# Kernel tuning notes

Hardware: AMD Instinct MI355X
Metric: run time of the kernel (lower is better)

Reference implementation:

```python
import jax, jax.numpy as jnp
import numpy as np

# Mamba2 hyperparams (from config['block'][0])
D_MODEL = 512
D_STATE = 64
D_CONV = 4
EXPAND = 2
HEADDIM = 64
D_INNER = EXPAND * D_MODEL          # 1024
NHEADS = D_INNER // HEADDIM         # 16
CONV_DIM = D_INNER + 2 * D_STATE    # 1152 (x, B, C share the depthwise conv)
D_IN_PROJ = 2 * D_INNER + 2 * D_STATE + NHEADS  # z | xBC | dt
EPS = 1e-5
BATCH, SEQLEN = 2, 4096


def setup_inputs() -> dict:
    key = jax.random.key(0)
    ks = jax.random.split(key, 10)
    x = jax.random.normal(ks[0], (BATCH, SEQLEN, D_MODEL), dtype=jnp.float32)
    W_in = jax.random.normal(ks[1], (D_MODEL, D_IN_PROJ), dtype=jnp.float32) * 0.02
    conv_w = jax.random.normal(ks[2], (CONV_DIM, 1, D_CONV), dtype=jnp.float32) * 0.2
    conv_b = jax.random.normal(ks[3], (CONV_DIM,), dtype=jnp.float32) * 0.02
    dt_bias = jax.random.uniform(ks[4], (NHEADS,), minval=-4.0, maxval=-1.0, dtype=jnp.float32)
    A_log = jnp.log(jax.random.uniform(ks[5], (NHEADS,), minval=1.0, maxval=16.0, dtype=jnp.float32))
    D = jax.random.normal(ks[6], (NHEADS,), dtype=jnp.float32) * 0.5 + 1.0
    norm_weight = jnp.ones((D_INNER,), dtype=jnp.float32)
    W_out = jax.random.normal(ks[7], (D_INNER, D_MODEL), dtype=jnp.float32) * 0.02
    return {"x": x, "W_in": W_in, "conv_w": conv_w, "conv_b": conv_b,
            "dt_bias": dt_bias, "A_log": A_log, "D": D,
            "norm_weight": norm_weight, "W_out": W_out}


def _mamba2_forward(x, W_in, conv_w, conv_b, dt_bias, A_log, D, norm_weight, W_out):
    b, l, _ = x.shape
    zxbcdt = x @ W_in                                      # (b, l, D_IN_PROJ)
    z = zxbcdt[..., :D_INNER]                              # gate branch
    xBC = zxbcdt[..., D_INNER:D_INNER + CONV_DIM]
    dt = zxbcdt[..., D_INNER + CONV_DIM:]                  # (b, l, h)

    # depthwise causal conv1d over sequence, then SiLU
    xBC_ncw = jnp.transpose(xBC, (0, 2, 1))                # (b, c, l)
    xBC_ncw = jax.lax.conv_general_dilated(
        xBC_ncw, conv_w, window_strides=(1,), padding=[(D_CONV - 1, 0)],
        dimension_numbers=("NCW", "OIW", "NCW"), feature_group_count=CONV_DIM)
    xBC_ncw = xBC_ncw + conv_b[None, :, None]
    xBC = jax.nn.silu(jnp.transpose(xBC_ncw, (0, 2, 1)))   # (b, l, c)

    x_ssm = xBC[..., :D_INNER].reshape(b, l, NHEADS, HEADDIM)  # (b,l,h,p)
    B = xBC[..., D_INNER:D_INNER + D_STATE]                    # (b,l,n)
    C = xBC[..., D_INNER + D_STATE:]                           # (b,l,n)

    dt = jax.nn.softplus(dt + dt_bias)                     # (b,l,h)
    A = -jnp.exp(A_log)                                    # (h,)
    dA = jnp.exp(dt * A)                                   # (b,l,h) discrete decay

    # selective scan: state s has shape (b, h, p, n)
    def step(s, inp):
        dA_t, dt_t, x_t, B_t, C_t = inp                    # (b,h),(b,h),(b,h,p),(b,n),(b,n)
        dBx = (dt_t[..., None] * x_t)[..., None] * B_t[:, None, None, :]
        s = s * dA_t[..., None, None] + dBx
        y_t = jnp.einsum("bhpn,bn->bhp", s, C_t)
        return s, y_t

    s0 = jnp.zeros((b, NHEADS, HEADDIM, D_STATE), dtype=x.dtype)
    xs = (jnp.moveaxis(dA, 1, 0), jnp.moveaxis(dt, 1, 0),
          jnp.moveaxis(x_ssm, 1, 0), jnp.moveaxis(B, 1, 0), jnp.moveaxis(C, 1, 0))
    _, ys = jax.lax.scan(step, s0, xs)                     # ys: (l,b,h,p)
    y = jnp.moveaxis(ys, 0, 1)                             # (b,l,h,p)

    y = y + D[None, None, :, None] * x_ssm                 # skip term
    y = y.reshape(b, l, D_INNER)

    # gated RMSNorm (norm after gating, mamba2 default)
    y = y * jax.nn.silu(z)
    var = jnp.mean(jnp.square(y), axis=-1, keepdims=True)
    y = y * jax.lax.rsqrt(var + EPS) * norm_weight

    return y @ W_out                                       # (b, l, d_model)


def reference(x, W_in, conv_w, conv_b, dt_bias, A_log, D, norm_weight, W_out):
    return _mamba2_forward(x, W_in, conv_w, conv_b, dt_bias, A_log, D, norm_weight, W_out)
```

## Files before the change

### kernel.cpp

```cpp
#include <hip/hip_runtime.h>
#include <hip/hip_bf16.h>

#define BATCH   2
#define SEQ     4096
#define DMODEL  512
#define DINNER  1024
#define DSTATE  64
#define NHEADS  16
#define HEADDIM 64
#define CONVDIM 1152
#define NPROJ   2192
#define NPROJ_PAD 2304
#define MROWS   (BATCH*SEQ)
#define QCH     64
#define NCHUNK  (SEQ/QCH)

typedef short bf16x8 __attribute__((ext_vector_type(8)));
typedef float f32x4  __attribute__((ext_vector_type(4)));
using bf16 = __hip_bfloat16;
typedef unsigned short ushort_t;
typedef unsigned int   uint_t;

__device__ __forceinline__ float sigmoidf_(float x) { return 1.f / (1.f + __expf(-x)); }
__device__ __forceinline__ float bf2f(ushort_t u) { return __uint_as_float((uint_t)u << 16); }
__device__ __forceinline__ ushort_t f2bfu(float f) {
    bf16 h = __float2bfloat16(f);
    return *(ushort_t*)&h;
}
__device__ __forceinline__ void bf8_to_f(const ushort_t* __restrict__ p, float* __restrict__ f) {
    uint4 u = *(const uint4*)p;
    f[0] = __uint_as_float((u.x & 0xFFFFu) << 16);
    f[1] = __uint_as_float(u.x & 0xFFFF0000u);
    f[2] = __uint_as_float((u.y & 0xFFFFu) << 16);
    f[3] = __uint_as_float(u.y & 0xFFFF0000u);
    f[4] = __uint_as_float((u.z & 0xFFFFu) << 16);
    f[5] = __uint_as_float(u.z & 0xFFFF0000u);
    f[6] = __uint_as_float((u.w & 0xFFFFu) << 16);
    f[7] = __uint_as_float(u.w & 0xFFFF0000u);
}
__device__ __forceinline__ uint4 f8_to_bf(const float* __restrict__ f) {
    union { ushort_t s[8]; uint4 u; } r;
#pragma unroll
    for (int i = 0; i < 8; i++) r.s[i] = f2bfu(f[i]);
    return r.u;
}

__device__ __forceinline__ void gload_lds16(const ushort_t* g, ushort_t* l)
{
    __builtin_amdgcn_global_load_lds(
        (const __attribute__((address_space(1))) void*)g,
        (__attribute__((address_space(3)))       void*)l,
        16, 0, 0);
}

__global__ __launch_bounds__(256, 4)
void prep_k(const float* __restrict__ x, ushort_t* __restrict__ xb,
            const float* __restrict__ W_in, ushort_t* __restrict__ WinT,
            const float* __restrict__ W_out, ushort_t* __restrict__ WoutT,
            const float* __restrict__ nw)
{
    __shared__ __align__(16) ushort_t tile[32][33];
    const int bid = blockIdx.x, tid = threadIdx.x;
    if (bid < 2048) {
        int i = bid * 256 + tid;
        float f[8];
        *(float4*)(f + 0) = ((const float4*)x)[i * 2 + 0];
        *(float4*)(f + 4) = ((const float4*)x)[i * 2 + 1];
        ((uint4*)xb)[i] = f8_to_bf(f);
        return;
    }
    const int tx = tid & 31, ty = tid >> 5;
    const float* in; ushort_t* out; int R, C, Cpad; const float* sv;
    int bx, by;
    if (bid < 3200) {
        int b2 = bid - 2048;
        bx = b2 % (NPROJ_PAD / 32); by = b2 / (NPROJ_PAD / 32);
        in = W_in; out = WinT; R = DMODEL; C = NPROJ; Cpad = NPROJ_PAD; sv = nullptr;
    } else {
        int b3 = bid - 3200;
        bx = b3 % (DMODEL / 32); by = b3 / (DMODEL / 32);
        in = W_out; out = WoutT; R = DINNER; C = DMODEL; Cpad = DMODEL; sv = nw;
    }
    int c0 = bx * 32, r0 = by * 32;
#pragma unroll
    for (int i = 0; i < 32; i += 8) {
        int r = r0 + ty + i, c = c0 + tx;
        float v = (r < R && c < C) ? in[(size_t)r * C + c] : 0.f;
        if (sv && r < R) v *= sv[r];
        tile[ty + i][tx] = f2bfu(v);
    }
    __syncthreads();
#pragma unroll
    for (int i = 0; i < 32; i += 8) {
        int orow = c0 + ty + i, ocol = r0 + tx;
        if (orow < Cpad && ocol < R) out[(size_t)orow * R + ocol] = tile[tx][ty + i];
    }
}

__global__ __launch_bounds__(256, 4)
void conv_k(const ushort_t* __restrict__ xpbc, const ushort_t* __restrict__ xpre,
            const float* __restrict__ cw, const float* __restrict__ cb,
            ushort_t* __restrict__ bcc, ushort_t* __restrict__ xs)
{
    const int bid = blockIdx.x, tid = threadIdx.x;
    if (bid < 512) {
        int idx = bid * 256 + tid;
        int row = idx >> 4, c8 = (idx & 15) * 8;
        int l = row & (SEQ - 1);
        float acc[8];
#pragma unroll
        for (int i = 0; i < 8; i++) acc[i] = cb[1024 + c8 + i];
#pragma unroll
        for (int j = 0; j < 4; j++) {
            int ll = l - 3 + j;
            if (ll >= 0) {
                float v[8];
                bf8_to_f(xpbc + (size_t)(row - 3 + j) * 128 + c8, v);
#pragma unroll
                for (int i = 0; i < 8; i++) acc[i] += cw[(1024 + c8 + i) * 4 + j] * v[i];
            }
        }
#pragma unroll
        for (int i = 0; i < 8; i++) { float v = acc[i]; acc[i] = v * sigmoidf_(v); }
        *(uint4*)(bcc + (size_t)row * 128 + c8) = f8_to_bf(acc);
        return;
    }
    const int b2 = bid - 512;
    const int gx = b2 & 127, b = b2 >> 7;
    const int c8 = (tid & 127) * 8;
    const int rh = tid >> 7;
    const int l0 = gx * 32 + rh * 16;
    float w[4][8], cbv[8];
#pragma unroll
    for (int i = 0; i < 8; i++) {
        cbv[i] = cb[c8 + i];
        float4 wv = *(const float4*)(cw + (size_t)(c8 + i) * 4);
        w[0][i] = wv.x; w[1][i] = wv.y; w[2][i] = wv.z; w[3][i] = wv.w;
    }
    float win[3][8];
#pragma unroll
    for (int j = 0; j < 3; j++) {
        int ll = l0 - 3 + j;
        if (ll >= 0) bf8_to_f(xpre + ((size_t)b * SEQ + ll) * 1024 + c8, win[j]);
        else {
#pragma unroll
            for (int i = 0; i < 8; i++) win[j][i] = 0.f;
        }
    }
#pragma unroll 4
    for (int r = 0; r < 16; r++) {
        int l = l0 + r;
        float cur[8], o[8];
        bf8_to_f(xpre + ((size_t)b * SEQ + l) * 1024 + c8, cur);
#pragma unroll
        for (int i = 0; i < 8; i++) {
            float a = cbv[i] + w[0][i] * win[0][i] + w[1][i] * win[1][i]
                             + w[2][i] * win[2][i] + w[3][i] * cur[i];
            o[i] = a * sigmoidf_(a);
        }
        *(uint4*)(xs + ((size_t)b * SEQ + l) * 1024 + c8) = f8_to_bf(o);
#pragma unroll
        for (int i = 0; i < 8; i++) { win[0][i] = win[1][i]; win[1][i] = win[2][i]; win[2][i] = cur[i]; }
    }
}

template<int MODE>
__global__ __launch_bounds__(256, MODE == 1 ? 4 : 3)
void gemm_k(const ushort_t* __restrict__ A, const ushort_t* __restrict__ Bt,
            ushort_t* __restrict__ zbuf, ushort_t* __restrict__ xpx,
            ushort_t* __restrict__ xpbc, float* __restrict__ dtv,
            float* __restrict__ dalog, const float* __restrict__ dt_b,
            const float* __restrict__ A_log, float* __restrict__ outf,
            int M, int N, int K)
{
    constexpr int TN = (MODE == 1) ? 64 : 128;
    constexpr int NJ = TN / 32;
    constexpr int SC = 132;
    constexpr int SMEM_ELTS = (MODE == 1) ? (128 * 64 + TN * 64) : (128 * SC);
    __shared__ __align__(16) ushort_t smem[SMEM_ELTS];
    ushort_t* As = smem;
    ushort_t* Bs = smem + 128 * 64;
    ushort_t* Cs = smem;

    const int tid  = threadIdx.x;
    const int wave = tid >> 6, lane = tid & 63;
    const int quad = lane >> 4, l16 = lane & 15;
    const int wm = (wave >> 1) * 64, wn = (wave & 1) * (TN / 2);

    const int GX = gridDim.x;
    int lin = blockIdx.y * GX + blockIdx.x;
    const int cpx = (GX * gridDim.y) >> 3;
    lin = (lin & 7) * cpx + (lin >> 3);
    const int m0 = (lin / GX) * 128, n0 = (lin % GX) * TN;

    const int srow = lane >> 3;
    const int scol = (lane & 7) * 8;
    const ushort_t* ag = A  + (size_t)(m0 + wave * 32       + srow) * K + scol;
    const ushort_t* bg = Bt + (size_t)(n0 + wave * (TN / 4) + srow) * K + scol;
    ushort_t* al = As + wave * 32 * 64;
    ushort_t* bl = Bs + wave * (TN / 4) * 64;

    f32x4 acc[4][NJ];
#pragma unroll
    for (int i = 0; i < 4; i++)
#pragma unroll
        for (int j = 0; j < NJ; j++) acc[i][j] = (f32x4){0.f, 0.f, 0.f, 0.f};
    float ssq4[4] = {0.f, 0.f, 0.f, 0.f};

    for (int k0 = 0; k0 < K; k0 += 64) {
        __syncthreads();
#pragma unroll
        for (int j = 0; j < 4; j++)
            gload_lds16(ag + (size_t)(j * 8) * K + k0, al + j * 8 * 64);
#pragma unroll
        for (int j = 0; j < NJ; j++)
            gload_lds16(bg + (size_t)(j * 8) * K + k0, bl + j * 8 * 64);
        __syncthreads();
#pragma unroll
        for (int kk = 0; kk < 64; kk += 32) {
            bf16x8 af[4], bfr[NJ];
#pragma unroll
            for (int i = 0; i < 4; i++)
                af[i] = *(const bf16x8*)(&As[(wm + i * 16 + l16) * 64 + kk + quad * 8]);
#pragma unroll
            for (int j = 0; j < NJ; j++)
                bfr[j] = *(const bf16x8*)(&Bs[(wn + j * 16 + l16) * 64 + kk + quad * 8]);
#pragma unroll
            for (int i = 0; i < 4; i++)
#pragma unroll
                for (int j = 0; j < NJ; j++)
                    acc[i][j] = __builtin_amdgcn_mfma_f32_16x16x32_bf16(af[i], bfr[j], acc[i][j], 0, 0, 0);
            if (MODE == 1 && (wave & 1) == 0) {
#pragma unroll
                for (int i = 0; i < 4; i++)
#pragma unroll
                    for (int e = 0; e < 8; e++) {
                        float f = bf2f((ushort_t)af[i][e]);
                        ssq4[i] += f * f;
                    }
            }
        }
    }
    if (MODE == 1) {
        __syncthreads();
        float* smemf = (float*)smem;
        if ((wave & 1) == 0) {
#pragma unroll
            for (int i = 0; i < 4; i++) {
                float s = ssq4[i];
                s += __shfl_xor(s, 16, 64);
                s += __shfl_xor(s, 32, 64);
                if (quad == 0) smemf[wm + i * 16 + l16] = s;
            }
        }
        __syncthreads();
#pragma unroll
        for (int i = 0; i < 4; i++)
#pragma unroll
            for (int j = 0; j < NJ; j++) {
                int col  = n0 + wn + j * 16 + l16;
                int rowl = wm + i * 16 + quad * 4;
#pragma unroll
                for (int r = 0; r < 4; r++) {
                    float sc = rsqrtf(smemf[rowl + r] * (1.f / DINNER) + 1e-5f);
                    outf[(size_t)(m0 + rowl + r) * N + col] = acc[i][j][r] * sc;
                }
            }
    } else if (n0 == 2176) {
#pragma unroll
        for (int i = 0; i < 4; i++)
#pragma unroll
            for (int j = 0; j < NJ; j++) {
                int col = n0 + wn + j * 16 + l16;
                int rowb = m0 + wm + i * 16 + quad * 4;
                if (col < N) {
                    int hh = col - 2176;
#pragma unroll
                    for (int r = 0; r < 4; r++) {
                        float v = acc[i][j][r];
                        size_t g = (size_t)hh * MROWS + (rowb + r);
                        float raw = v + dt_b[hh];
                        float sp  = (raw > 20.f) ? raw : log1pf(__expf(raw));
                        dtv  [g] = sp;
                        dalog[g] = -__expf(A_log[hh]) * sp;
                    }
                }
            }
    } else {
        __syncthreads();
#pragma unroll
        for (int i = 0; i < 4; i++)
#pragma unroll
            for (int j = 0; j < NJ; j++)
#pragma unroll
                for (int r = 0; r < 4; r++)
                    Cs[(wm + i * 16 + quad * 4 + r) * SC + wn + j * 16 + l16] = f2bfu(acc[i][j][r]);
        __syncthreads();
        ushort_t* dst; int ld, coff;
        if (n0 < 1024)      { dst = zbuf; ld = 1024; coff = n0; }
        else if (n0 < 2048) { dst = xpx;  ld = 1024; coff = n0 - 1024; }
        else                { dst = xpbc; ld = 128;  coff = 0; }
#pragma unroll
        for (int jj = 0; jj < 8; jj++) {
            int idx = jj * 256 + tid;
            int row = idx >> 4, cq = (idx & 15) * 8;
            uint4 v = *(const uint4*)&Cs[row * SC + cq];
            *(uint4*)&dst[(size_t)(m0 + row) * ld + coff + cq] = v;
        }
    }
}

__global__ __launch_bounds__(256, 3)
void chunk_state_k(const ushort_t* __restrict__ xs, const ushort_t* __restrict__ bcc,
                   const float* __restrict__ dtv, const float* __restrict__ dalog,
                   ushort_t* __restrict__ statesT, float* __restrict__ cdecay)
{
    const int c = blockIdx.x, h = blockIdx.y, b = blockIdx.z;
    __shared__ __align__(16) ushort_t xsT[64 * 72];
    __shared__ __align__(16) ushort_t BwT[64 * 72];
    __shared__ float wc[64];
    const int tid = threadIdx.x;
    const int ts = tid >> 2, q4 = (tid & 3) * 16;
    const int l = c * QCH + ts;
    const int tswz = ts ^ ((tid & 3) << 4);
    if (tid < 64) {
        size_t gl = (size_t)h * MROWS + (size_t)b * SEQ + c * QCH + tid;
        float v = dalog[gl];
#pragma unroll
        for (int off = 1; off < 64; off <<= 1) {
            float u = __shfl_up(v, off, 64);
            if (tid >= off) v += u;
        }
        float tot = __shfl(v, 63, 64);
        wc[tid] = __expf(tot - v) * dtv[gl];
        if (tid == 63) cdecay[(c * BATCH + b) * NHEADS + h] = __expf(tot);
    }
    {
        const int ch0 = h * HEADDIM + q4;
        const ushort_t* rp = xs + ((size_t)b * SEQ + l) * 1024 + ch0;
        union { uint4 u; ushort_t s[8]; } u0, u1;
        u0.u = *(const uint4*)rp; u1.u = *(const uint4*)(rp + 8);
#pragma unroll
        for (int i = 0; i < 8; i++) {
            xsT[(q4 + i) * 72 + tswz]     = u0.s[i];
            xsT[(q4 + 8 + i) * 72 + tswz] = u1.s[i];
        }
    }
    __syncthreads();
    {
        float bv[16];
        const ushort_t* rp = bcc + ((size_t)b * SEQ + l) * 128;
        bf8_to_f(rp + q4, bv); bf8_to_f(rp + q4 + 8, bv + 8);
        const float wt = wc[ts];
#pragma unroll
        for (int i = 0; i < 16; i++) BwT[(q4 + i) * 72 + tswz] = f2bfu(bv[i] * wt);
    }
    __syncthreads();
    const int wave = tid >> 6, lane = tid & 63;
    const int quad = lane >> 4, l16 = lane & 15;
    f32x4 acc[4];
#pragma unroll
    for (int j = 0; j < 4; j++) acc[j] = (f32x4){0.f, 0.f, 0.f, 0.f};
#pragma unroll
    for (int kk = 0; kk < 64; kk += 32) {
        bf16x8 af = *(const bf16x8*)(&xsT[(wave * 16 + l16) * 72 + ((kk + quad * 8) ^ ((wave & 3) << 4))]);
#pragma unroll
        for (int j = 0; j < 4; j++) {
            bf16x8 bf_ = *(const bf16x8*)(&BwT[(j * 16 + l16) * 72 + ((kk + quad * 8) ^ ((j & 3) << 4))]);
            acc[j] = __builtin_amdgcn_mfma_f32_16x16x32_bf16(af, bf_, acc[j], 0, 0, 0);
        }
    }
    ushort_t* base = statesT + ((size_t)(c * BATCH + b) * NHEADS + h) * (HEADDIM * DSTATE);
#pragma unroll
    for (int j = 0; j < 4; j++)
#pragma unroll
        for (int r = 0; r < 4; r++)
            base[(wave * 16 + quad * 4 + r) * 64 + j * 16 + l16] = f2bfu(acc[j][r]);
}

__global__ void scan_combine_k(ushort_t* __restrict__ states, const float* __restrict__ cdecay)
{
    const int blk = blockIdx.x;
    const int eighth = blk & 7;
    const int h = (blk >> 3) & 15;
    const int b = blk >> 7;
    const int tid = threadIdx.x;
    __shared__ float dec[64];
    if (tid < 64) dec[tid] = cdecay[(tid * BATCH + b) * NHEADS + h];
    __syncthreads();
    const size_t cstride = (size_t)BATCH * NHEADS * HEADDIM * DSTATE;
    ushort_t* base = states + ((size_t)b * NHEADS + h) * (HEADDIM * DSTATE) + eighth * 512 + tid * 4;
    float sx = 0.f, sy = 0.f, sz = 0.f, sw = 0.f;
    uint2 pre[4];
#pragma unroll
    for (int j = 0; j < 4; j++) pre[j] = *(const uint2*)(base + j * cstride);
    for (int c = 0; c < NCHUNK; c++) {
        uint2 Sc = pre[c & 3];
        if (c + 4 < NCHUNK) pre[c & 3] = *(const uint2*)(base + (size_t)(c + 4) * cstride);
        float d = dec[c];
        uint2 o;
        o.x = (uint_t)f2bfu(sx) | ((uint_t)f2bfu(sy) << 16);
        o.y = (uint_t)f2bfu(sz) | ((uint_t)f2bfu(sw) << 16);
        *(uint2*)(base + (size_t)c * cstride) = o;
        sx = d * sx + __uint_as_float((Sc.x & 0xFFFFu) << 16);
        sy = d * sy + __uint_as_float(Sc.x & 0xFFFF0000u);
        sz = d * sz + __uint_as_float((Sc.y & 0xFFFFu) << 16);
        sw = d * sw + __uint_as_float(Sc.y & 0xFFFF0000u);
    }
}

__global__ __launch_bounds__(256, 3)
void chunk_y_k(const ushort_t* __restrict__ xs, const ushort_t* __restrict__ bcc,
               ushort_t* zio,
               const float* __restrict__ dtv, const float* __restrict__ dalog,
               const ushort_t* __restrict__ statesT, const float* __restrict__ Dp)
{
    const int c = blockIdx.x, h = blockIdx.y, b = blockIdx.z;
    __shared__ __align__(16) ushort_t CLb [64 * 72];
    __shared__ __align__(16) ushort_t BLb [64 * 72];
    __shared__ __align__(16) ushort_t xsT [64 * 72];
    __shared__ __align__(16) ushort_t attL[64 * 72];
    __shared__ float cum[64], wdt[64];
    const int tid = threadIdx.x;
    const int ts = tid >> 2, q4 = (tid & 3) * 16;
    const int l = c * QCH + ts;
    const int tswz = ts ^ ((tid & 3) << 4);
    const float Dh = Dp[h];
    {
        const int ch0 = h * HEADDIM + q4;
        const ushort_t* rp = xs + ((size_t)b * SEQ + l) * 1024 + ch0;
        union { uint4 u; ushort_t s[8]; } u0, u1;
        u0.u = *(const uint4*)rp; u1.u = *(const uint4*)(rp + 8);
#pragma unroll
        for (int i = 0; i < 8; i++) {
            xsT[(q4 + i) * 72 + tswz]     = u0.s[i];
            xsT[(q4 + 8 + i) * 72 + tswz] = u1.s[i];
        }
    }
    {
        const ushort_t* rp = bcc + ((size_t)b * SEQ + l) * 128;
        *(uint4*)&BLb[ts * 72 + q4]     = *(const uint4*)(rp + q4);
        *(uint4*)&BLb[ts * 72 + q4 + 8] = *(const uint4*)(rp + q4 + 8);
        *(uint4*)&CLb[ts * 72 + q4]     = *(const uint4*)(rp + 64 + q4);
        *(uint4*)&CLb[ts * 72 + q4 + 8] = *(const uint4*)(rp + 64 + q4 + 8);
    }
    if (tid < 64) {
        size_t gl = (size_t)h * MROWS + (size_t)b * SEQ + c * QCH + tid;
        float v = dalog[gl];
#pragma unroll
        for (int off = 1; off < 64; off <<= 1) {
            float u = __shfl_up(v, off, 64);
            if (tid >= off) v += u;
        }
        cum[tid] = v;
        wdt[tid] = dtv[gl];
    }
    __syncthreads();
    const int wave = tid >> 6, lane = tid & 63;
    const int quad = lane >> 4, l16 = lane & 15;
    {
        f32x4 sacc[4];
#pragma unroll
        for (int j = 0; j < 4; j++) sacc[j] = (f32x4){0.f, 0.f, 0.f, 0.f};
#pragma unroll
        for (int kk = 0; kk < 64; kk += 32) {
            bf16x8 af = *(const bf16x8*)(&CLb[(wave * 16 + l16) * 72 + kk + quad * 8]);
#pragma unroll
            for (int j = 0; j < 4; j++) {
                bf16x8 bf_ = *(const bf16x8*)(&BLb[(j * 16 + l16) * 72 + kk + quad * 8]);
                sacc[j] = __builtin_amdgcn_mfma_f32_16x16x32_bf16(af, bf_, sacc[j], 0, 0, 0);
            }
        }
#pragma unroll
        for (int r = 0; r < 4; r++) {
            const int t = wave * 16 + quad * 4 + r;
            const float ct = cum[t];
#pragma unroll
            for (int j = 0; j < 4; j++) {
                const int s = j * 16 + l16;
                float a = (s <= t) ? sacc[j][r] * __expf(ct - cum[s]) * wdt[s] : 0.f;
                attL[t * 72 + s] = f2bfu(a);
            }
        }
    }
    {
        f32x4 accY[4], accI[4];
#pragma unroll
        for (int j = 0; j < 4; j++) { accY[j] = (f32x4){0.f, 0.f, 0.f, 0.f}; accI[j] = (f32x4){0.f, 0.f, 0.f, 0.f}; }
        const ushort_t* spg = statesT + ((size_t)(c * BATCH + b) * NHEADS + h) * (HEADDIM * DSTATE);
#pragma unroll
        for (int kk = 0; kk < 64; kk += 32) {
            bf16x8 a2 = *(const bf16x8*)(&attL[(wave * 16 + l16) * 72 + kk + quad * 8]);
            bf16x8 a3 = *(const bf16x8*)(&CLb [(wave * 16 + l16) * 72 + kk + quad * 8]);
#pragma unroll
            for (int j = 0; j < 4; j++) {
                bf16x8 b2 = *(const bf16x8*)(&xsT[(j * 16 + l16) * 72 + ((kk + quad * 8) ^ ((j & 3) << 4))]);
                accY[j] = __builtin_amdgcn_mfma_f32_16x16x32_bf16(a2, b2, accY[j], 0, 0, 0);
                bf16x8 b3 = *(const bf16x8*)(spg + (j * 16 + l16) * 64 + kk + quad * 8);
                accI[j] = __builtin_amdgcn_mfma_f32_16x16x32_bf16(a3, b3, accI[j], 0, 0, 0);
            }
        }
        __syncthreads();
#pragma unroll
        for (int r = 0; r < 4; r++) {
            const int t = wave * 16 + quad * 4 + r;
            const float et = __expf(cum[t]);
#pragma unroll
            for (int j = 0; j < 4; j++) {
                const int p = j * 16 + l16;
                float xv = bf2f(xsT[p * 72 + (t ^ ((j & 3) << 4))]);
                float y = accY[j][r] + et * accI[j][r] + Dh * xv;
                BLb[t * 72 + p] = f2bfu(y);
            }
        }
    }
    {
        ushort_t* zrow = zio + ((size_t)b * SEQ + l) * DINNER + h * HEADDIM + q4;
        float zv[16], yv[16], o[16];
        bf8_to_f(zrow, zv); bf8_to_f(zrow + 8, zv + 8);
        bf8_to_f(&BLb[ts * 72 + q4], yv); bf8_to_f(&BLb[ts * 72 + q4 + 8], yv + 8);
#pragma unroll
        for (int j = 0; j < 16; j++) {
            float z = zv[j];
            o[j] = yv[j] * z * sigmoidf_(z);
        }
        *(uint4*)(zrow)     = f8_to_bf(o);
        *(uint4*)(zrow + 8) = f8_to_bf(o + 8);
    }
}

extern "C" void kernel_launch(void* const* d_in, const int* in_sizes, int n_in,
                              void* d_out, int out_size, void* d_ws, size_t ws_size,
                              hipStream_t stream)
{
    const float* x      = (const float*)d_in[0];
    const float* W_in   = (const float*)d_in[1];
    const float* conv_w = (const float*)d_in[2];
    const float* conv_b = (const float*)d_in[3];
    const float* dt_b   = (const float*)d_in[4];
    const float* A_log  = (const float*)d_in[5];
    const float* Dp     = (const float*)d_in[6];
    const float* nw     = (const float*)d_in[7];
    const float* W_out  = (const float*)d_in[8];
    float* out = (float*)d_out;

    char* w = (char*)d_ws;
    ushort_t* zbuf    = (ushort_t*)(w);
    ushort_t* xs      = (ushort_t*)(w + 16777216);
    ushort_t* xpre    = (ushort_t*)(w + 33554432);
    ushort_t* statesT = (ushort_t*)(w + 33554432);
    char* dscr = (char*)d_out;
    ushort_t* xpbc  = (ushort_t*)(dscr);
    float*    dtv   = (float*)(dscr + 2097152);
    float*    dalog = (float*)(dscr + 2621440);
    float*    cdec  = (float*)(dscr + 3145728);
    ushort_t* WinT  = (ushort_t*)(dscr + 4194304);
    ushort_t* bcc   = (ushort_t*)(dscr + 4194304);
    ushort_t* WoutT = (ushort_t*)(dscr + 6815744);
    ushort_t* xb    = (ushort_t*)(dscr + 8388608);

    prep_k<<<2048 + (NPROJ_PAD / 32) * (DMODEL / 32) + (DMODEL / 32) * (DINNER / 32), 256, 0, stream>>>(
        x, xb, W_in, WinT, W_out, WoutT, nw);
    gemm_k<0><<<dim3(NPROJ_PAD / 128, MROWS / 128), 256, 0, stream>>>(
        xb, WinT, zbuf, xpre, xpbc, dtv, dalog, dt_b, A_log, nullptr,
        MROWS, NPROJ, DMODEL);
    conv_k<<<512 + 256, 256, 0, stream>>>(xpbc, xpre, conv_w, conv_b, bcc, xs);
    chunk_state_k<<<dim3(NCHUNK, NHEADS, BATCH), 256, 0, stream>>>(
        xs, bcc, dtv, dalog, statesT, cdec);
    scan_combine_k<<<BATCH * NHEADS * 8, 128, 0, stream>>>(statesT, cdec);
    chunk_y_k<<<dim3(NCHUNK, NHEADS, BATCH), 256, 0, stream>>>(
        xs, bcc, zbuf, dtv, dalog, statesT, Dp);
    gemm_k<1><<<dim3(DMODEL / 64, MROWS / 128), 256, 0, stream>>>(
        zbuf, WoutT, nullptr, nullptr, nullptr, nullptr, nullptr, nullptr,
        nullptr, out, MROWS, DMODEL, DINNER);
}
```

Baseline: 206.3 us.

## Replace input-projection GEMM with 256x128 triple-buffered LDS-pipelined kernel

The input projection GEMM moves to a new 512-thread kernel with 256x128 tiles. It keeps three LDS stages in flight, with async global-to-LDS prefetch two k-steps ahead interleaved between MFMA phases. It also raises wave priority around the MFMA bursts. The aim is to hide global load latency and improve data reuse per block. In exchange it runs one block per CU with about 147KB of LDS, which can leave a tail wave imbalance across 576 blocks with only 8 k-iterations. The output GEMM is split into its own non-templated kernel with no change in behaviour.

```diff
diff --git a/kernel.cpp b/kernel.cpp
--- a/kernel.cpp
+++ b/kernel.cpp
@@ -164,113 +164,99 @@
     }
 }
 
-template<int MODE>
-__global__ __launch_bounds__(256, MODE == 1 ? 4 : 3)
-void gemm_k(const ushort_t* __restrict__ A, const ushort_t* __restrict__ Bt,
-            ushort_t* __restrict__ zbuf, ushort_t* __restrict__ xpx,
-            ushort_t* __restrict__ xpbc, float* __restrict__ dtv,
-            float* __restrict__ dalog, const float* __restrict__ dt_b,
-            const float* __restrict__ A_log, float* __restrict__ outf,
-            int M, int N, int K)
-{
-    constexpr int TN = (MODE == 1) ? 64 : 128;
-    constexpr int NJ = TN / 32;
-    constexpr int SC = 132;
-    constexpr int SMEM_ELTS = (MODE == 1) ? (128 * 64 + TN * 64) : (128 * SC);
-    __shared__ __align__(16) ushort_t smem[SMEM_ELTS];
-    ushort_t* As = smem;
-    ushort_t* Bs = smem + 128 * 64;
-    ushort_t* Cs = smem;
+#define G8_BM 256
+#define G8_BN 128
+#define G8_BK 64
+#define G8_BUFE (G8_BM * G8_BK + G8_BN * G8_BK)
+
+__global__ __launch_bounds__(512, 1)
+void gemm8_k(const ushort_t* __restrict__ A, const ushort_t* __restrict__ Bt,
+             ushort_t* __restrict__ zbuf, ushort_t* __restrict__ xpx,
+             ushort_t* __restrict__ xpbc, float* __restrict__ dtv,
+             float* __restrict__ dalog, const float* __restrict__ dt_b,
+             const float* __restrict__ A_log, int M, int N, int K)
+{
+    __shared__ __align__(16) ushort_t smem8[3 * G8_BUFE];
 
     const int tid  = threadIdx.x;
     const int wave = tid >> 6, lane = tid & 63;
     const int quad = lane >> 4, l16 = lane & 15;
-    const int wm = (wave >> 1) * 64, wn = (wave & 1) * (TN / 2);
+    const int wm = (wave >> 2) * 128;
+    const int wn = (wave & 3) * 32;
 
     const int GX = gridDim.x;
     int lin = blockIdx.y * GX + blockIdx.x;
     const int cpx = (GX * gridDim.y) >> 3;
     lin = (lin & 7) * cpx + (lin >> 3);
-    const int m0 = (lin / GX) * 128, n0 = (lin % GX) * TN;
-
-    const int srow = lane >> 3;
-    const int scol = (lane & 7) * 8;
-    const ushort_t* ag = A  + (size_t)(m0 + wave * 32       + srow) * K + scol;
-    const ushort_t* bg = Bt + (size_t)(n0 + wave * (TN / 4) + srow) * K + scol;
-    ushort_t* al = As + wave * 32 * 64;
-    ushort_t* bl = Bs + wave * (TN / 4) * 64;
-
-    f32x4 acc[4][NJ];
-#pragma unroll
-    for (int i = 0; i < 4; i++)
-#pragma unroll
-        for (int j = 0; j < NJ; j++) acc[i][j] = (f32x4){0.f, 0.f, 0.f, 0.f};
-    float ssq4[4] = {0.f, 0.f, 0.f, 0.f};
-
-    for (int k0 = 0; k0 < K; k0 += 64) {
-        __syncthreads();
-#pragma unroll
-        for (int j = 0; j < 4; j++)
-            gload_lds16(ag + (size_t)(j * 8) * K + k0, al + j * 8 * 64);
-#pragma unroll
-        for (int j = 0; j < NJ; j++)
-            gload_lds16(bg + (size_t)(j * 8) * K + k0, bl + j * 8 * 64);
-        __syncthreads();
-#pragma unroll
-        for (int kk = 0; kk < 64; kk += 32) {
-            bf16x8 af[4], bfr[NJ];
-#pragma unroll
-            for (int i = 0; i < 4; i++)
-                af[i] = *(const bf16x8*)(&As[(wm + i * 16 + l16) * 64 + kk + quad * 8]);
-#pragma unroll
-            for (int j = 0; j < NJ; j++)
-                bfr[j] = *(const bf16x8*)(&Bs[(wn + j * 16 + l16) * 64 + kk + quad * 8]);
-#pragma unroll
-            for (int i = 0; i < 4; i++)
-#pragma unroll
-                for (int j = 0; j < NJ; j++)
-                    acc[i][j] = __builtin_amdgcn_mfma_f32_16x16x32_bf16(af[i], bfr[j], acc[i][j], 0, 0, 0);
-            if (MODE == 1 && (wave & 1) == 0) {
-#pragma unroll
-                for (int i = 0; i < 4; i++)
-#pragma unroll
-                    for (int e = 0; e < 8; e++) {
-                        float f = bf2f((ushort_t)af[i][e]);
-                        ssq4[i] += f * f;
-                    }
-            }
-        }
-    }
-    if (MODE == 1) {
-        __syncthreads();
-        float* smemf = (float*)smem;
-        if ((wave & 1) == 0) {
-#pragma unroll
-            for (int i = 0; i < 4; i++) {
-                float s = ssq4[i];
-                s += __shfl_xor(s, 16, 64);
-                s += __shfl_xor(s, 32, 64);
-                if (quad == 0) smemf[wm + i * 16 + l16] = s;
-            }
-        }
-        __syncthreads();
-#pragma unroll
-        for (int i = 0; i < 4; i++)
-#pragma unroll
-            for (int j = 0; j < NJ; j++) {
-                int col  = n0 + wn + j * 16 + l16;
-                int rowl = wm + i * 16 + quad * 4;
-#pragma unroll
-                for (int r = 0; r < 4; r++) {
-                    float sc = rsqrtf(smemf[rowl + r] * (1.f / DINNER) + 1e-5f);
-                    outf[(size_t)(m0 + rowl + r) * N + col] = acc[i][j][r] * sc;
-                }
-            }
-    } else if (n0 == 2176) {
-#pragma unroll
-        for (int i = 0; i < 4; i++)
-#pragma unroll
-            for (int j = 0; j < NJ; j++) {
+    const int m0 = (lin / GX) * G8_BM, n0 = (lin % GX) * G8_BN;
+
+    const int srow = lane >> 3, scol = (lane & 7) * 8;
+    const ushort_t* agBase = A  + (size_t)(m0 + wave * 16 + srow) * K + scol;
+    const ushort_t* bgBase = Bt + (size_t)(n0 + wave * 16 + srow) * K + scol;
+
+    auto stage_unit = [&](int kt, int u) {
+        ushort_t* dst = smem8 + (kt % 3) * G8_BUFE
+                      + (u == 2 ? (G8_BM * G8_BK) : u * (128 * 64))
+                      + wave * 16 * 64;
+        const ushort_t* src = (u == 2 ? bgBase : agBase + (size_t)(u * 128) * K)
+                            + (size_t)kt * G8_BK;
+        gload_lds16(src, dst);
+        gload_lds16(src + (size_t)8 * K, dst + 8 * 64);
+    };
+
+    f32x4 acc[8][2];
+#pragma unroll
+    for (int i = 0; i < 8; i++)
+#pragma unroll
+        for (int j = 0; j < 2; j++) acc[i][j] = (f32x4){0.f, 0.f, 0.f, 0.f};
+
+    const int NKT = K / G8_BK;
+#pragma unroll
+    for (int u = 0; u < 3; u++) stage_unit(0, u);
+#pragma unroll
+    for (int u = 0; u < 3; u++) stage_unit(1, u);
+
+    for (int kt = 0; kt < NKT; kt++) {
+        asm volatile("s_waitcnt vmcnt(6)" ::: "memory");
+        __builtin_amdgcn_s_barrier();
+        const ushort_t* As_ = smem8 + (kt % 3) * G8_BUFE;
+        const ushort_t* Bs_ = As_ + G8_BM * G8_BK;
+        const bool pf = (kt < NKT - 2);
+#pragma unroll
+        for (int ih = 0; ih < 2; ih++) {
+            bf16x8 afr[4][2];
+#pragma unroll
+            for (int ii = 0; ii < 4; ii++)
+#pragma unroll
+                for (int kk = 0; kk < 2; kk++)
+                    afr[ii][kk] = *(const bf16x8*)(&As_[(wm + (ih * 4 + ii) * 16 + l16) * 64 + kk * 32 + quad * 8]);
+#pragma unroll
+            for (int jh = 0; jh < 2; jh++) {
+                bf16x8 bfr[2];
+#pragma unroll
+                for (int kk = 0; kk < 2; kk++)
+                    bfr[kk] = *(const bf16x8*)(&Bs_[(wn + jh * 16 + l16) * 64 + kk * 32 + quad * 8]);
+                const int ph = ih * 2 + jh;
+                if (pf && ph < 3) stage_unit(kt + 2, ph);
+                __builtin_amdgcn_s_barrier();
+                __builtin_amdgcn_s_setprio(1);
+#pragma unroll
+                for (int ii = 0; ii < 4; ii++)
+#pragma unroll
+                    for (int kk = 0; kk < 2; kk++)
+                        acc[ih * 4 + ii][jh] = __builtin_amdgcn_mfma_f32_16x16x32_bf16(
+                            afr[ii][kk], bfr[kk], acc[ih * 4 + ii][jh], 0, 0, 0);
+                __builtin_amdgcn_s_setprio(0);
+                __builtin_amdgcn_s_barrier();
+            }
+        }
+    }
+    __syncthreads();
+    if (n0 == 2176) {
+#pragma unroll
+        for (int i = 0; i < 8; i++)
+#pragma unroll
+            for (int j = 0; j < 2; j++) {
                 int col = n0 + wn + j * 16 + l16;
                 int rowb = m0 + wm + i * 16 + quad * 4;
                 if (col < N) {
@@ -287,14 +273,14 @@
                 }
             }
     } else {
-        __syncthreads();
-#pragma unroll
-        for (int i = 0; i < 4; i++)
-#pragma unroll
-            for (int j = 0; j < NJ; j++)
+        ushort_t* Cs = smem8;
+#pragma unroll
+        for (int i = 0; i < 8; i++)
+#pragma unroll
+            for (int j = 0; j < 2; j++)
 #pragma unroll
                 for (int r = 0; r < 4; r++)
-                    Cs[(wm + i * 16 + quad * 4 + r) * SC + wn + j * 16 + l16] = f2bfu(acc[i][j][r]);
+                    Cs[(wm + i * 16 + quad * 4 + r) * 132 + wn + j * 16 + l16] = f2bfu(acc[i][j][r]);
         __syncthreads();
         ushort_t* dst; int ld, coff;
         if (n0 < 1024)      { dst = zbuf; ld = 1024; coff = n0; }
@@ -302,12 +288,107 @@
         else                { dst = xpbc; ld = 128;  coff = 0; }
 #pragma unroll
         for (int jj = 0; jj < 8; jj++) {
-            int idx = jj * 256 + tid;
+            int idx = jj * 512 + tid;
             int row = idx >> 4, cq = (idx & 15) * 8;
-            uint4 v = *(const uint4*)&Cs[row * SC + cq];
+            uint4 v = *(const uint4*)&Cs[row * 132 + cq];
             *(uint4*)&dst[(size_t)(m0 + row) * ld + coff + cq] = v;
         }
     }
+}
+
+__global__ __launch_bounds__(256, 4)
+void gemm1_k(const ushort_t* __restrict__ A, const ushort_t* __restrict__ Bt,
+             float* __restrict__ outf, int M, int N, int K)
+{
+    constexpr int TN = 64;
+    constexpr int NJ = TN / 32;
+    __shared__ __align__(16) ushort_t smem[128 * 64 + TN * 64];
+    ushort_t* As = smem;
+    ushort_t* Bs = smem + 128 * 64;
+
+    const int tid  = threadIdx.x;
+    const int wave = tid >> 6, lane = tid & 63;
+    const int quad = lane >> 4, l16 = lane & 15;
+    const int wm = (wave >> 1) * 64, wn = (wave & 1) * (TN / 2);
+
+    const int GX = gridDim.x;
+    int lin = blockIdx.y * GX + blockIdx.x;
+    const int cpx = (GX * gridDim.y) >> 3;
+    lin = (lin & 7) * cpx + (lin >> 3);
+    const int m0 = (lin / GX) * 128, n0 = (lin % GX) * TN;
+
+    const int srow = lane >> 3;
+    const int scol = (lane & 7) * 8;
+    const ushort_t* ag = A  + (size_t)(m0 + wave * 32       + srow) * K + scol;
+    const ushort_t* bg = Bt + (size_t)(n0 + wave * (TN / 4) + srow) * K + scol;
+    ushort_t* al = As + wave * 32 * 64;
+    ushort_t* bl = Bs + wave * (TN / 4) * 64;
+
+    f32x4 acc[4][NJ];
+#pragma unroll
+    for (int i = 0; i < 4; i++)
+#pragma unroll
+        for (int j = 0; j < NJ; j++) acc[i][j] = (f32x4){0.f, 0.f, 0.f, 0.f};
+    float ssq4[4] = {0.f, 0.f, 0.f, 0.f};
+
+    for (int k0 = 0; k0 < K; k0 += 64) {
+        __syncthreads();
+#pragma unroll
+        for (int j = 0; j < 4; j++)
+            gload_lds16(ag + (size_t)(j * 8) * K + k0, al + j * 8 * 64);
+#pragma unroll
+        for (int j = 0; j < NJ; j++)
+            gload_lds16(bg + (size_t)(j * 8) * K + k0, bl + j * 8 * 64);
+        __syncthreads();
+#pragma unroll
+        for (int kk = 0; kk < 64; kk += 32) {
+            bf16x8 af[4], bfr[NJ];
+#pragma unroll
+            for (int i = 0; i < 4; i++)
+                af[i] = *(const bf16x8*)(&As[(wm + i * 16 + l16) * 64 + kk + quad * 8]);
+#pragma unroll
+            for (int j = 0; j < NJ; j++)
+                bfr[j] = *(const bf16x8*)(&Bs[(wn + j * 16 + l16) * 64 + kk + quad * 8]);
+#pragma unroll
+            for (int i = 0; i < 4; i++)
+#pragma unroll
+                for (int j = 0; j < NJ; j++)
+                    acc[i][j] = __builtin_amdgcn_mfma_f32_16x16x32_bf16(af[i], bfr[j], acc[i][j], 0, 0, 0);
+            if ((wave & 1) == 0) {
+#pragma unroll
+                for (int i = 0; i < 4; i++)
+#pragma unroll
+                    for (int e = 0; e < 8; e++) {
+                        float f = bf2f((ushort_t)af[i][e]);
+                        ssq4[i] += f * f;
+                    }
+            }
+        }
+    }
+    __syncthreads();
+    float* smemf = (float*)smem;
+    if ((wave & 1) == 0) {
+#pragma unroll
+        for (int i = 0; i < 4; i++) {
+            float s = ssq4[i];
+            s += __shfl_xor(s, 16, 64);
+            s += __shfl_xor(s, 32, 64);
+            if (quad == 0) smemf[wm + i * 16 + l16] = s;
+        }
+    }
+    __syncthreads();
+#pragma unroll
+    for (int i = 0; i < 4; i++)
+#pragma unroll
+        for (int j = 0; j < NJ; j++) {
+            int col  = n0 + wn + j * 16 + l16;
+            int rowl = wm + i * 16 + quad * 4;
+#pragma unroll
+            for (int r = 0; r < 4; r++) {
+                float sc = rsqrtf(smemf[rowl + r] * (1.f / DINNER) + 1e-5f);
+                outf[(size_t)(m0 + rowl + r) * N + col] = acc[i][j][r] * sc;
+            }
+        }
 }
 
 __global__ __launch_bounds__(256, 3)
@@ -561,8 +642,8 @@
 
     prep_k<<<2048 + (NPROJ_PAD / 32) * (DMODEL / 32) + (DMODEL / 32) * (DINNER / 32), 256, 0, stream>>>(
         x, xb, W_in, WinT, W_out, WoutT, nw);
-    gemm_k<0><<<dim3(NPROJ_PAD / 128, MROWS / 128), 256, 0, stream>>>(
-        xb, WinT, zbuf, xpre, xpbc, dtv, dalog, dt_b, A_log, nullptr,
+    gemm8_k<<<dim3(NPROJ_PAD / G8_BN, MROWS / G8_BM), 512, 0, stream>>>(
+        xb, WinT, zbuf, xpre, xpbc, dtv, dalog, dt_b, A_log,
         MROWS, NPROJ, DMODEL);
     conv_k<<<512 + 256, 256, 0, stream>>>(xpbc, xpre, conv_w, conv_b, bcc, xs);
     chunk_state_k<<<dim3(NCHUNK, NHEADS, BATCH), 256, 0, stream>>>(
@@ -570,7 +651,6 @@
     scan_combine_k<<<BATCH * NHEADS * 8, 128, 0, stream>>>(statesT, cdec);
     chunk_y_k<<<dim3(NCHUNK, NHEADS, BATCH), 256, 0, stream>>>(
         xs, bcc, zbuf, dtv, dalog, statesT, Dp);
-    gemm_k<1><<<dim3(DMODEL / 64, MROWS / 128), 256, 0, stream>>>(
-        zbuf, WoutT, nullptr, nullptr, nullptr, nullptr, nullptr, nullptr,
-        nullptr, out, MROWS, DMODEL, DINNER);
-}
+    gemm1_k<<<dim3(DMODEL / 64, MROWS / 128), 256, 0, stream>>>(
+        zbuf, WoutT, out, MROWS, DMODEL, DINNER);
+}
```

New measurement: 235.6 us. 14.2% more time.

## Fuse depthwise conv+SiLU for x channels into in-proj GEMM epilogue

Applied to the files above, without the earlier changes.

The in-projection GEMM epilogue now applies the causal depthwise conv and SiLU directly from the shared-memory output tile for the x channels, writing xs instead of a pre-conv buffer. Only the 3 leading and 3 trailing rows of each 128-row tile are saved to a small boundary buffer. The conv kernel's x path shrinks to recomputing the first 3 rows of each tile from those boundary rows. This removes a full write and re-read of the pre-conv x activation, at the cost of a heavier GEMM epilogue with extra register use.

```diff
diff --git a/kernel.cpp b/kernel.cpp
--- a/kernel.cpp
+++ b/kernel.cpp
@@ -14,6 +14,7 @@
 #define MROWS   (BATCH*SEQ)
 #define QCH     64
 #define NCHUNK  (SEQ/QCH)
+#define NMT     (MROWS/128)
 
 typedef short bf16x8 __attribute__((ext_vector_type(8)));
 typedef float f32x4  __attribute__((ext_vector_type(4)));
@@ -98,7 +99,7 @@
 }
 
 __global__ __launch_bounds__(256, 4)
-void conv_k(const ushort_t* __restrict__ xpbc, const ushort_t* __restrict__ xpre,
+void conv_k(const ushort_t* __restrict__ xpbc, const ushort_t* __restrict__ xbnd,
             const float* __restrict__ cw, const float* __restrict__ cb,
             ushort_t* __restrict__ bcc, ushort_t* __restrict__ xs)
 {
@@ -125,53 +126,43 @@
         *(uint4*)(bcc + (size_t)row * 128 + c8) = f8_to_bf(acc);
         return;
     }
-    const int b2 = bid - 512;
-    const int gx = b2 & 127, b = b2 >> 7;
-    const int c8 = (tid & 127) * 8;
-    const int rh = tid >> 7;
-    const int l0 = gx * 32 + rh * 16;
-    float w[4][8], cbv[8];
-#pragma unroll
-    for (int i = 0; i < 8; i++) {
-        cbv[i] = cb[c8 + i];
-        float4 wv = *(const float4*)(cw + (size_t)(c8 + i) * 4);
-        w[0][i] = wv.x; w[1][i] = wv.y; w[2][i] = wv.z; w[3][i] = wv.w;
-    }
-    float win[3][8];
-#pragma unroll
-    for (int j = 0; j < 3; j++) {
-        int ll = l0 - 3 + j;
-        if (ll >= 0) bf8_to_f(xpre + ((size_t)b * SEQ + ll) * 1024 + c8, win[j]);
-        else {
-#pragma unroll
-            for (int i = 0; i < 8; i++) win[j][i] = 0.f;
-        }
-    }
-#pragma unroll 4
-    for (int r = 0; r < 16; r++) {
-        int l = l0 + r;
-        float cur[8], o[8];
-        bf8_to_f(xpre + ((size_t)b * SEQ + l) * 1024 + c8, cur);
-#pragma unroll
-        for (int i = 0; i < 8; i++) {
-            float a = cbv[i] + w[0][i] * win[0][i] + w[1][i] * win[1][i]
-                             + w[2][i] * win[2][i] + w[3][i] * cur[i];
-            o[i] = a * sigmoidf_(a);
-        }
-        *(uint4*)(xs + ((size_t)b * SEQ + l) * 1024 + c8) = f8_to_bf(o);
-#pragma unroll
-        for (int i = 0; i < 8; i++) { win[0][i] = win[1][i]; win[1][i] = win[2][i]; win[2][i] = cur[i]; }
-    }
+    int idx = (bid - 512) * 256 + tid;
+    const int c8 = (idx & 127) * 8;
+    const int rowid = idx >> 7;
+    const int mt = rowid / 3, t = rowid - mt * 3;
+    const int l = (mt * 128 + t) & (SEQ - 1);
+    float acc[8];
+#pragma unroll
+    for (int i = 0; i < 8; i++) acc[i] = cb[c8 + i];
+#pragma unroll
+    for (int j = 0; j < 4; j++) {
+        int ll = l - 3 + j;
+        if (ll >= 0) {
+            int tapidx = t - 3 + j;
+            const ushort_t* src = (tapidx >= 0)
+                ? &xbnd[((size_t)mt * 6 + tapidx) * 1024 + c8]
+                : &xbnd[((size_t)(mt - 1) * 6 + tapidx + 6) * 1024 + c8];
+            float v[8];
+            bf8_to_f(src, v);
+#pragma unroll
+            for (int i = 0; i < 8; i++) acc[i] += cw[(c8 + i) * 4 + j] * v[i];
+        }
+    }
+    float o[8];
+#pragma unroll
+    for (int i = 0; i < 8; i++) { float v = acc[i]; o[i] = v * sigmoidf_(v); }
+    *(uint4*)(xs + ((size_t)mt * 128 + t) * 1024 + c8) = f8_to_bf(o);
 }
 
 template<int MODE>
 __global__ __launch_bounds__(256, MODE == 1 ? 4 : 3)
 void gemm_k(const ushort_t* __restrict__ A, const ushort_t* __restrict__ Bt,
-            ushort_t* __restrict__ zbuf, ushort_t* __restrict__ xpx,
-            ushort_t* __restrict__ xpbc, float* __restrict__ dtv,
-            float* __restrict__ dalog, const float* __restrict__ dt_b,
-            const float* __restrict__ A_log, float* __restrict__ outf,
-            int M, int N, int K)
+            ushort_t* __restrict__ zbuf, ushort_t* __restrict__ xs,
+            ushort_t* __restrict__ xbnd, ushort_t* __restrict__ xpbc,
+            float* __restrict__ dtv, float* __restrict__ dalog,
+            const float* __restrict__ dt_b, const float* __restrict__ A_log,
+            const float* __restrict__ cw, const float* __restrict__ cb,
+            float* __restrict__ outf, int M, int N, int K)
 {
     constexpr int TN = (MODE == 1) ? 64 : 128;
     constexpr int NJ = TN / 32;
@@ -296,16 +287,52 @@
                 for (int r = 0; r < 4; r++)
                     Cs[(wm + i * 16 + quad * 4 + r) * SC + wn + j * 16 + l16] = f2bfu(acc[i][j][r]);
         __syncthreads();
-        ushort_t* dst; int ld, coff;
-        if (n0 < 1024)      { dst = zbuf; ld = 1024; coff = n0; }
-        else if (n0 < 2048) { dst = xpx;  ld = 1024; coff = n0 - 1024; }
-        else                { dst = xpbc; ld = 128;  coff = 0; }
-#pragma unroll
-        for (int jj = 0; jj < 8; jj++) {
-            int idx = jj * 256 + tid;
-            int row = idx >> 4, cq = (idx & 15) * 8;
-            uint4 v = *(const uint4*)&Cs[row * SC + cq];
-            *(uint4*)&dst[(size_t)(m0 + row) * ld + coff + cq] = v;
+        if (MODE == 0 && n0 >= 1024 && n0 < 2048) {
+            const int cq  = (tid & 15) * 8;
+            const int gch = (n0 - 1024) + cq;
+            const int mt  = m0 >> 7;
+            float wv[4][8], cbv[8];
+#pragma unroll
+            for (int i = 0; i < 8; i++) {
+                cbv[i] = cb[gch + i];
+                float4 w4 = *(const float4*)(cw + (size_t)(gch + i) * 4);
+                wv[0][i] = w4.x; wv[1][i] = w4.y; wv[2][i] = w4.z; wv[3][i] = w4.w;
+            }
+#pragma unroll
+            for (int jj = 0; jj < 8; jj++) {
+                int row = jj * 16 + (tid >> 4);
+                if (row < 3)
+                    *(uint4*)&xbnd[((size_t)mt * 6 + row) * 1024 + gch] =
+                        *(const uint4*)&Cs[row * SC + cq];
+                else if (row >= 125)
+                    *(uint4*)&xbnd[((size_t)mt * 6 + (row - 122)) * 1024 + gch] =
+                        *(const uint4*)&Cs[row * SC + cq];
+                if (row >= 3) {
+                    float v0[8], v1[8], v2[8], v3[8], o[8];
+                    bf8_to_f(&Cs[(row - 3) * SC + cq], v0);
+                    bf8_to_f(&Cs[(row - 2) * SC + cq], v1);
+                    bf8_to_f(&Cs[(row - 1) * SC + cq], v2);
+                    bf8_to_f(&Cs[(row    ) * SC + cq], v3);
+#pragma unroll
+                    for (int i = 0; i < 8; i++) {
+                        float a = cbv[i] + wv[0][i] * v0[i] + wv[1][i] * v1[i]
+                                         + wv[2][i] * v2[i] + wv[3][i] * v3[i];
+                        o[i] = a * sigmoidf_(a);
+                    }
+                    *(uint4*)&xs[(size_t)(m0 + row) * 1024 + gch] = f8_to_bf(o);
+                }
+            }
+        } else {
+            ushort_t* dst; int ld, coff;
+            if (n0 < 1024) { dst = zbuf; ld = 1024; coff = n0; }
+            else           { dst = xpbc; ld = 128;  coff = 0; }
+#pragma unroll
+            for (int jj = 0; jj < 8; jj++) {
+                int idx = jj * 256 + tid;
+                int row = idx >> 4, cq = (idx & 15) * 8;
+                uint4 v = *(const uint4*)&Cs[row * SC + cq];
+                *(uint4*)&dst[(size_t)(m0 + row) * ld + coff + cq] = v;
+            }
         }
     }
 }
@@ -547,7 +574,7 @@
     char* w = (char*)d_ws;
     ushort_t* zbuf    = (ushort_t*)(w);
     ushort_t* xs      = (ushort_t*)(w + 16777216);
-    ushort_t* xpre    = (ushort_t*)(w + 33554432);
+    ushort_t* xbnd    = (ushort_t*)(w + 33554432);
     ushort_t* statesT = (ushort_t*)(w + 33554432);
     char* dscr = (char*)d_out;
     ushort_t* xpbc  = (ushort_t*)(dscr);
@@ -562,9 +589,9 @@
     prep_k<<<2048 + (NPROJ_PAD / 32) * (DMODEL / 32) + (DMODEL / 32) * (DINNER / 32), 256, 0, stream>>>(
         x, xb, W_in, WinT, W_out, WoutT, nw);
     gemm_k<0><<<dim3(NPROJ_PAD / 128, MROWS / 128), 256, 0, stream>>>(
-        xb, WinT, zbuf, xpre, xpbc, dtv, dalog, dt_b, A_log, nullptr,
-        MROWS, NPROJ, DMODEL);
-    conv_k<<<512 + 256, 256, 0, stream>>>(xpbc, xpre, conv_w, conv_b, bcc, xs);
+        xb, WinT, zbuf, xs, xbnd, xpbc, dtv, dalog, dt_b, A_log, conv_w, conv_b,
+        nullptr, MROWS, NPROJ, DMODEL);
+    conv_k<<<512 + 96, 256, 0, stream>>>(xpbc, xbnd, conv_w, conv_b, bcc, xs);
     chunk_state_k<<<dim3(NCHUNK, NHEADS, BATCH), 256, 0, stream>>>(
         xs, bcc, dtv, dalog, statesT, cdec);
     scan_combine_k<<<BATCH * NHEADS * 8, 128, 0, stream>>>(statesT, cdec);
@@ -572,5 +599,5 @@
         xs, bcc, zbuf, dtv, dalog, statesT, Dp);
     gemm_k<1><<<dim3(DMODEL / 64, MROWS / 128), 256, 0, stream>>>(
         zbuf, WoutT, nullptr, nullptr, nullptr, nullptr, nullptr, nullptr,
-        nullptr, out, MROWS, DMODEL, DINNER);
-}
+        nullptr, nullptr, nullptr, nullptr, out, MROWS, DMODEL, DINNER);
+}
```

After: 207.8 us. No clear change (+0.7%).
